# Kernel tuning notes

Measured on AMD Instinct MI355X. Metric: run time of the kernel, lower is better.

Reference implementation:

```python
import jax, jax.numpy as jnp
import numpy as np

NUM_ROUTES = 1152
NUM_CAPS = 10
CAPS_IN = 8
CAPS_DIM = 16
BATCH = 128
NUM_IT = 3


def _squash(s):
    # s: [..., caps_dim]; scale = |s|^2 / ((1+|s|^2) * |s|)
    sqn = jnp.sum(s * s, axis=-1, keepdims=True)
    return s * (sqn / ((1.0 + sqn) * jnp.sqrt(sqn)))


def setup_inputs() -> dict:
    key = jax.random.key(0)
    k1, k2 = jax.random.split(key)
    x = jax.random.normal(k1, (BATCH, NUM_ROUTES, CAPS_IN), dtype=jnp.float32)
    W = jax.random.normal(k2, (1, NUM_ROUTES, NUM_CAPS, CAPS_DIM, CAPS_IN), dtype=jnp.float32)
    return {"input": x, "W": W}


def reference(input, W):
    # u_hat[b,r,j,d] = W[r,j,d,c] @ x[b,r,c]  (original broadcasts W over batch)
    u_hat = jnp.einsum('rjdc,brc->brjd', W[0], input)
    r, j = u_hat.shape[1], u_hat.shape[2]
    b_ij = jnp.zeros((r, j), dtype=u_hat.dtype)  # shared across batch, as in original
    v = None
    for _ in range(NUM_IT):
        c_ij = jax.nn.softmax(b_ij, axis=1)          # softmax over num_caps (dim=2 orig)
        s = jnp.einsum('rj,brjd->bjd', c_ij, u_hat)  # weighted sum over routes
        v = _squash(s)                                # [bs, num_caps, caps_dim]
        # agreement: <u_hat, v> averaged over batch (original updates every iter)
        b_ij = b_ij + jnp.mean(jnp.einsum('brjd,bjd->brj', u_hat, v), axis=0)
    return v[..., None]  # [bs, num_caps, caps_dim, 1], matches v_j.squeeze(1) shape
```

## Files before the change

### kernel.cpp

```cpp
#include <hip/hip_runtime.h>
#include <math.h>

#define R_ROUTES 1152
#define N_CAPS 10
#define C_IN 8
#define D_DIM 16
#define B_BATCH 128
#define JD 160
#define KK 9216
#define KSPLIT 48
#define RS 24
#define NG 5
#define BH 2
#define NBLK (KSPLIT * NG * BH)

typedef __attribute__((ext_vector_type(8))) short short8;
typedef __attribute__((ext_vector_type(4))) float f32x4;

__device__ inline unsigned short f2bf(float f) {
    unsigned int u = __float_as_uint(f);
    unsigned int r = u + 0x7FFFu + ((u >> 16) & 1u);
    return (unsigned short)(r >> 16);
}
__device__ inline float bf2f(unsigned short h) {
    return __uint_as_float(((unsigned int)h) << 16);
}


__global__ __launch_bounds__(256) void k_zero(f32x4* __restrict__ p) {
    int i = blockIdx.x * 256 + threadIdx.x;
    p[i] = (f32x4){0.f, 0.f, 0.f, 0.f};
}

template <bool FIRST>
__device__ inline void iter_body(
    const float* __restrict__ x, const float* __restrict__ W,
    const float* __restrict__ ctab, float* __restrict__ s,
    int ks, int ng, int bh, int t) {
    int r0 = ks * RS, jd0 = ng * 32, b_base = bh * 64;
    int w = t >> 6, l = t & 63, row = l & 15, quad = l >> 4;
    const float* px = x + (size_t)(b_base + w * 16 + row) * KK + ks * 192;
    f32x4 acc0 = {0,0,0,0}, acc1 = {0,0,0,0};
#pragma unroll
    for (int st = 0; st < 6; st++) {
        int rr = r0 + st * 4 + quad;
        float c0 = FIRST ? 0.1f : ctab[rr * N_CAPS + (jd0 >> 4)];
        float c1 = FIRST ? 0.1f : ctab[rr * N_CAPS + (jd0 >> 4) + 1];
        const float4* wp0 = (const float4*)(W + ((size_t)rr * JD + jd0 + row) * C_IN);
        const float4* wp1 = (const float4*)(W + ((size_t)rr * JD + jd0 + 16 + row) * C_IN);
        float4 wa = wp0[0], wb = wp0[1], wc = wp1[0], wd = wp1[1];
        float wv0[8] = {wa.x,wa.y,wa.z,wa.w, wb.x,wb.y,wb.z,wb.w};
        float wv1[8] = {wc.x,wc.y,wc.z,wc.w, wd.x,wd.y,wd.z,wd.w};
        short8 Bh0, Bh1;
#pragma unroll
        for (int i = 0; i < 8; i++) {
            Bh0[i] = (short)f2bf(wv0[i] * c0);
            Bh1[i] = (short)f2bf(wv1[i] * c1);
        }
        float4 x0 = *(const float4*)(px + st * 32 + quad * 8);
        float4 x1 = *(const float4*)(px + st * 32 + quad * 8 + 4);
        float xv[8] = {x0.x,x0.y,x0.z,x0.w, x1.x,x1.y,x1.z,x1.w};
        short8 Ah, Al;
#pragma unroll
        for (int i = 0; i < 8; i++) {
            unsigned short h = f2bf(xv[i]);
            Ah[i] = (short)h;
            Al[i] = (short)f2bf(xv[i] - bf2f(h));
        }
        acc0 = __builtin_amdgcn_mfma_f32_16x16x32_bf16(Ah, Bh0, acc0, 0, 0, 0);
        acc0 = __builtin_amdgcn_mfma_f32_16x16x32_bf16(Al, Bh0, acc0, 0, 0, 0);
        acc1 = __builtin_amdgcn_mfma_f32_16x16x32_bf16(Ah, Bh1, acc1, 0, 0, 0);
        acc1 = __builtin_amdgcn_mfma_f32_16x16x32_bf16(Al, Bh1, acc1, 0, 0, 0);
    }
#pragma unroll
    for (int i = 0; i < 4; i++) {
        int b0 = b_base + w * 16 + quad * 4 + i;
        atomicAdd(&s[(size_t)b0 * JD + jd0 + row],      acc0[i]);
        atomicAdd(&s[(size_t)b0 * JD + jd0 + 16 + row], acc1[i]);
    }
}

__global__ __launch_bounds__(256) void k_first(
    const float* __restrict__ x, const float* __restrict__ W,
    unsigned short* __restrict__ xT, float* __restrict__ s0,
    f32x4* __restrict__ z12) {
    __shared__ float tile[32][33];
    int id = blockIdx.x, t = threadIdx.x;

    if (id < NBLK) {
        iter_body<true>(x, W, nullptr, s0, id % KSPLIT, (id / KSPLIT) % NG,
                        id / (KSPLIT * NG), t);
        return;
    }
    if (id < NBLK + 288) {
        int bx = id - NBLK;
        int tx = t & 31, ty = t >> 5;
        for (int by = 0; by < 4; by++) {
            if (by) __syncthreads();
#pragma unroll
            for (int i = 0; i < 4; i++) {
                int row = ty + i * 8;
                tile[row][tx] = x[(size_t)(by * 32 + row) * KK + bx * 32 + tx];
            }
            __syncthreads();
#pragma unroll
            for (int i = 0; i < 4; i++) {
                int row = ty + i * 8;
                xT[(size_t)(bx * 32 + row) * B_BATCH + by * 32 + tx] = f2bf(tile[tx][row]);
            }
        }
        return;
    }
    int idx = (id - (NBLK + 288)) * 256 + t;
    z12[idx] = (f32x4){0.f, 0.f, 0.f, 0.f};
}

__global__ __launch_bounds__(256) void k_iter(
    const float* __restrict__ x, const float* __restrict__ W,
    const float* __restrict__ ctab, float* __restrict__ s) {
    iter_body<false>(x, W, ctab, s, blockIdx.x, blockIdx.y, blockIdx.z,
                     threadIdx.x);
}

template <int ACCUM>
__global__ __launch_bounds__(256) void k_va(
    const unsigned short* __restrict__ xT, const float* __restrict__ s_prev,
    const float* __restrict__ W, float* __restrict__ b_ij,
    float* __restrict__ ctab) {
    __shared__ unsigned short vb[JD][136];
    __shared__ float bnew[4][N_CAPS];
    int t = threadIdx.x;
    int r0 = blockIdx.x * 4, rc0 = blockIdx.x * 32;

#pragma unroll
    for (int q = 0; q < 5; q++) {
        int pi = t * 5 + q;
        int b = pi / N_CAPS, j = pi % N_CAPS;
        const float4* sp4 = (const float4*)(s_prev + (size_t)b * JD + j * D_DIM);
        float4 a0 = sp4[0], a1 = sp4[1], a2 = sp4[2], a3 = sp4[3];
        float sv[D_DIM] = {a0.x,a0.y,a0.z,a0.w, a1.x,a1.y,a1.z,a1.w,
                           a2.x,a2.y,a2.z,a2.w, a3.x,a3.y,a3.z,a3.w};
        float sqn = 0.f;
#pragma unroll
        for (int d = 0; d < D_DIM; d++) sqn = fmaf(sv[d], sv[d], sqn);
        float scale = sqn / ((1.f + sqn) * sqrtf(sqn));
#pragma unroll
        for (int d = 0; d < D_DIM; d++)
            vb[j * D_DIM + d][b] = f2bf(sv[d] * scale);
    }
    __syncthreads();

    int w = t >> 6, l = t & 63, row = l & 15, quad = l >> 4;
    int rhalf = l >> 5, cbase = (quad & 1) * 4;

    for (int u = w; u < 20; u += 4) {
        int mt = u / 10, nt = u % 10;
        const short8* pa = (const short8*)(xT + (size_t)(rc0 + mt * 16 + row) * B_BATCH);
        f32x4 acc = {0,0,0,0};
#pragma unroll
        for (int st = 0; st < 4; st++)
            acc = __builtin_amdgcn_mfma_f32_16x16x32_bf16(
                pa[st * 4 + quad],
                *(const short8*)&vb[nt * 16 + row][st * 32 + quad * 8],
                acc, 0, 0, 0);
        int r = r0 + 2 * mt + rhalf;
        const float* wp = W + ((size_t)r * JD + nt * 16 + row) * C_IN + cbase;
        float4 w4 = *(const float4*)wp;
        float part = acc[0]*w4.x + acc[1]*w4.y + acc[2]*w4.z + acc[3]*w4.w;
#pragma unroll
        for (int off = 1; off < 32; off <<= 1) part += __shfl_xor(part, off, 32);
        if ((l & 31) == 0) bnew[2 * mt + rhalf][nt] = part * (1.f / (float)B_BATCH);
    }
    __syncthreads();

    if (t < 4) {
        float bj[N_CAPS], m = -1e30f;
#pragma unroll
        for (int j = 0; j < N_CAPS; j++) {
            float base = ACCUM ? b_ij[(r0 + t) * N_CAPS + j] : 0.f;
            bj[j] = base + bnew[t][j];
            m = fmaxf(m, bj[j]);
        }
        if (!ACCUM) {
#pragma unroll
            for (int j = 0; j < N_CAPS; j++) b_ij[(r0 + t) * N_CAPS + j] = bj[j];
        }
        float sum = 0.f;
#pragma unroll
        for (int j = 0; j < N_CAPS; j++) { bj[j] = expf(bj[j] - m); sum += bj[j]; }
        float inv = 1.f / sum;
#pragma unroll
        for (int j = 0; j < N_CAPS; j++) ctab[(r0 + t) * N_CAPS + j] = bj[j] * inv;
    }
}

__global__ __launch_bounds__(320) void k_rs_final(
    const float* __restrict__ s, float* __restrict__ out) {
    int t = threadIdx.x;
    int bloc = t / JD, jd = t % JD;
    int b = blockIdx.x * 2 + bloc;
    float acc = s[(size_t)b * JD + jd];
    float sq = acc * acc;
#pragma unroll
    for (int off = 1; off < 16; off <<= 1) sq += __shfl_xor(sq, off, 16);
    float scale = sq / ((1.f + sq) * sqrtf(sq));
    out[(size_t)b * JD + jd] = acc * scale;
}

extern "C" void kernel_launch(void* const* d_in, const int* in_sizes, int n_in,
                              void* d_out, int out_size, void* d_ws, size_t ws_size,
                              hipStream_t stream) {
    const float* x = (const float*)d_in[0];
    const float* W = (const float*)d_in[1];
    float* out = (float*)d_out;
    char* ws = (char*)d_ws;

    float*          s0   = (float*)(ws + 0);
    float*          s1   = (float*)(ws + 81920);
    float*          s2   = (float*)(ws + 163840);
    float*          b_ij = (float*)(ws + 245760);
    float*          ctab = (float*)(ws + 291840);
    unsigned short* xT   = (unsigned short*)(ws + 337920);

    k_zero<<<20, 256, 0, stream>>>((f32x4*)s0);

    k_first<<<808, 256, 0, stream>>>(x, W, xT, s0, (f32x4*)s1);

    k_va<0><<<288, 256, 0, stream>>>(xT, s0, W, b_ij, ctab);

    k_iter<<<dim3(KSPLIT, NG, BH), 256, 0, stream>>>(x, W, ctab, s1);

    k_va<1><<<288, 256, 0, stream>>>(xT, s1, W, b_ij, ctab);

    k_iter<<<dim3(KSPLIT, NG, BH), 256, 0, stream>>>(x, W, ctab, s2);

    k_rs_final<<<64, 320, 0, stream>>>(s2, out);
}
```

Measured before the change: 112.0 us.

## Replace final atomics with per-split partial stores and fold zeroing into prep kernel

The last routing iteration now writes per-K-split partial sums to a separate buffer, and the final squash kernel reduces those 48 partials itself, so the third pass needs no atomics. The first iteration is split out of the fused transpose kernel into its own launch, and zeroing s0/s1 moves into the transpose kernel, which removes the separate zero launch. The k_va tile loop is also fully unrolled. The trade-off is extra memory traffic for the partial buffer and a serial 48-way read in the final kernel, plus an extra launch dependency because the transpose and the first iteration no longer run in one kernel.

Result: no change. 112.0 us (-0.0%).

```diff
diff --git a/kernel.cpp b/kernel.cpp
--- a/kernel.cpp
+++ b/kernel.cpp
@@ -12,7 +12,7 @@
 #define RS 24
 #define NG 5
 #define BH 2
-#define NBLK (KSPLIT * NG * BH)
+#define SPART 20480
 
 typedef __attribute__((ext_vector_type(8))) short short8;
 typedef __attribute__((ext_vector_type(4))) float f32x4;
@@ -27,16 +27,40 @@
 }
 
 
-__global__ __launch_bounds__(256) void k_zero(f32x4* __restrict__ p) {
-    int i = blockIdx.x * 256 + threadIdx.x;
-    p[i] = (f32x4){0.f, 0.f, 0.f, 0.f};
-}
-
-template <bool FIRST>
-__device__ inline void iter_body(
+__global__ __launch_bounds__(256) void k_prep0(
+    const float* __restrict__ x, unsigned short* __restrict__ xT,
+    f32x4* __restrict__ zbase) {
+    __shared__ float tile[32][33];
+    int id = blockIdx.x, t = threadIdx.x;
+    if (id < 288) {
+        int bx = id;
+        int tx = t & 31, ty = t >> 5;
+        for (int by = 0; by < 4; by++) {
+            if (by) __syncthreads();
+#pragma unroll
+            for (int i = 0; i < 4; i++) {
+                int row = ty + i * 8;
+                tile[row][tx] = x[(size_t)(by * 32 + row) * KK + bx * 32 + tx];
+            }
+            __syncthreads();
+#pragma unroll
+            for (int i = 0; i < 4; i++) {
+                int row = ty + i * 8;
+                xT[(size_t)(bx * 32 + row) * B_BATCH + by * 32 + tx] = f2bf(tile[tx][row]);
+            }
+        }
+        return;
+    }
+    int idx = (id - 288) * 256 + t;
+    zbase[idx] = (f32x4){0.f, 0.f, 0.f, 0.f};
+}
+
+template <int FIRST, int STORE>
+__global__ __launch_bounds__(256) void k_iter(
     const float* __restrict__ x, const float* __restrict__ W,
-    const float* __restrict__ ctab, float* __restrict__ s,
-    int ks, int ng, int bh, int t) {
+    const float* __restrict__ ctab, float* __restrict__ s) {
+    int t = threadIdx.x;
+    int ks = blockIdx.x, ng = blockIdx.y, bh = blockIdx.z;
     int r0 = ks * RS, jd0 = ng * 32, b_base = bh * 64;
     int w = t >> 6, l = t & 63, row = l & 15, quad = l >> 4;
     const float* px = x + (size_t)(b_base + w * 16 + row) * KK + ks * 192;
@@ -72,54 +96,22 @@
         acc1 = __builtin_amdgcn_mfma_f32_16x16x32_bf16(Ah, Bh1, acc1, 0, 0, 0);
         acc1 = __builtin_amdgcn_mfma_f32_16x16x32_bf16(Al, Bh1, acc1, 0, 0, 0);
     }
-#pragma unroll
-    for (int i = 0; i < 4; i++) {
-        int b0 = b_base + w * 16 + quad * 4 + i;
-        atomicAdd(&s[(size_t)b0 * JD + jd0 + row],      acc0[i]);
-        atomicAdd(&s[(size_t)b0 * JD + jd0 + 16 + row], acc1[i]);
-    }
-}
-
-__global__ __launch_bounds__(256) void k_first(
-    const float* __restrict__ x, const float* __restrict__ W,
-    unsigned short* __restrict__ xT, float* __restrict__ s0,
-    f32x4* __restrict__ z12) {
-    __shared__ float tile[32][33];
-    int id = blockIdx.x, t = threadIdx.x;
-
-    if (id < NBLK) {
-        iter_body<true>(x, W, nullptr, s0, id % KSPLIT, (id / KSPLIT) % NG,
-                        id / (KSPLIT * NG), t);
-        return;
-    }
-    if (id < NBLK + 288) {
-        int bx = id - NBLK;
-        int tx = t & 31, ty = t >> 5;
-        for (int by = 0; by < 4; by++) {
-            if (by) __syncthreads();
-#pragma unroll
-            for (int i = 0; i < 4; i++) {
-                int row = ty + i * 8;
-                tile[row][tx] = x[(size_t)(by * 32 + row) * KK + bx * 32 + tx];
-            }
-            __syncthreads();
-#pragma unroll
-            for (int i = 0; i < 4; i++) {
-                int row = ty + i * 8;
-                xT[(size_t)(bx * 32 + row) * B_BATCH + by * 32 + tx] = f2bf(tile[tx][row]);
-            }
-        }
-        return;
-    }
-    int idx = (id - (NBLK + 288)) * 256 + t;
-    z12[idx] = (f32x4){0.f, 0.f, 0.f, 0.f};
-}
-
-__global__ __launch_bounds__(256) void k_iter(
-    const float* __restrict__ x, const float* __restrict__ W,
-    const float* __restrict__ ctab, float* __restrict__ s) {
-    iter_body<false>(x, W, ctab, s, blockIdx.x, blockIdx.y, blockIdx.z,
-                     threadIdx.x);
+    if (STORE) {
+        float* sp = s + (size_t)ks * SPART;
+#pragma unroll
+        for (int i = 0; i < 4; i++) {
+            int b0 = b_base + w * 16 + quad * 4 + i;
+            sp[(size_t)b0 * JD + jd0 + row]      = acc0[i];
+            sp[(size_t)b0 * JD + jd0 + 16 + row] = acc1[i];
+        }
+    } else {
+#pragma unroll
+        for (int i = 0; i < 4; i++) {
+            int b0 = b_base + w * 16 + quad * 4 + i;
+            atomicAdd(&s[(size_t)b0 * JD + jd0 + row],      acc0[i]);
+            atomicAdd(&s[(size_t)b0 * JD + jd0 + 16 + row], acc1[i]);
+        }
+    }
 }
 
 template <int ACCUM>
@@ -153,7 +145,9 @@
     int w = t >> 6, l = t & 63, row = l & 15, quad = l >> 4;
     int rhalf = l >> 5, cbase = (quad & 1) * 4;
 
-    for (int u = w; u < 20; u += 4) {
+#pragma unroll
+    for (int jt = 0; jt < 5; jt++) {
+        int u = jt * 4 + w;
         int mt = u / 10, nt = u % 10;
         const short8* pa = (const short8*)(xT + (size_t)(rc0 + mt * 16 + row) * B_BATCH);
         f32x4 acc = {0,0,0,0};
@@ -194,12 +188,15 @@
     }
 }
 
-__global__ __launch_bounds__(320) void k_rs_final(
-    const float* __restrict__ s, float* __restrict__ out) {
+__global__ __launch_bounds__(320) void k_final(
+    const float* __restrict__ s2p, float* __restrict__ out) {
     int t = threadIdx.x;
     int bloc = t / JD, jd = t % JD;
     int b = blockIdx.x * 2 + bloc;
-    float acc = s[(size_t)b * JD + jd];
+    float acc = 0.f;
+#pragma unroll
+    for (int ks = 0; ks < KSPLIT; ks++)
+        acc += s2p[(size_t)ks * SPART + (size_t)b * JD + jd];
     float sq = acc * acc;
 #pragma unroll
     for (int off = 1; off < 16; off <<= 1) sq += __shfl_xor(sq, off, 16);
@@ -217,22 +214,22 @@
 
     float*          s0   = (float*)(ws + 0);
     float*          s1   = (float*)(ws + 81920);
-    float*          s2   = (float*)(ws + 163840);
-    float*          b_ij = (float*)(ws + 245760);
-    float*          ctab = (float*)(ws + 291840);
-    unsigned short* xT   = (unsigned short*)(ws + 337920);
-
-    k_zero<<<20, 256, 0, stream>>>((f32x4*)s0);
-
-    k_first<<<808, 256, 0, stream>>>(x, W, xT, s0, (f32x4*)s1);
+    float*          b_ij = (float*)(ws + 163840);
+    float*          ctab = (float*)(ws + 209920);
+    unsigned short* xT   = (unsigned short*)(ws + 256000);
+    float*          s2p  = (float*)(ws + 2615296);
+
+    k_prep0<<<328, 256, 0, stream>>>(x, xT, (f32x4*)ws);
+
+    k_iter<1, 0><<<dim3(KSPLIT, NG, BH), 256, 0, stream>>>(x, W, nullptr, s0);
 
     k_va<0><<<288, 256, 0, stream>>>(xT, s0, W, b_ij, ctab);
 
-    k_iter<<<dim3(KSPLIT, NG, BH), 256, 0, stream>>>(x, W, ctab, s1);
+    k_iter<0, 0><<<dim3(KSPLIT, NG, BH), 256, 0, stream>>>(x, W, ctab, s1);
 
     k_va<1><<<288, 256, 0, stream>>>(xT, s1, W, b_ij, ctab);
 
-    k_iter<<<dim3(KSPLIT, NG, BH), 256, 0, stream>>>(x, W, ctab, s2);
-
-    k_rs_final<<<64, 320, 0, stream>>>(s2, out);
-}
+    k_iter<0, 1><<<dim3(KSPLIT, NG, BH), 256, 0, stream>>>(x, W, ctab, s2p);
+
+    k_final<<<64, 320, 0, stream>>>(s2p, out);
+}
```
